# Kernel tuning notes

Hardware: AMD Instinct MI355X
Metric: run time of the kernel (lower is better)

The kernel has to match this reference:

```python
import jax, jax.numpy as jnp
import numpy as np

IRREPS = [(32, 0), (16, 1), (8, 2)]          # (multiplicity, l)
DIMS = [m * (2 * l + 1) for m, l in IRREPS]  # [32, 48, 40]
OFF = np.concatenate([[0], np.cumsum(DIMS)]).astype(int)
FEAT = int(OFF[-1])                          # 120
H = 4                                        # num_heads
EPS = 1e-5
N_NODES = 50000
N_EDGES = 800000


def split(x):
    # split last axis into per-irrep blocks [..., mul, 2l+1]
    return [x[..., OFF[i]:OFF[i + 1]].reshape(x.shape[:-1] + (m, 2 * l + 1))
            for i, (m, l) in enumerate(IRREPS)]


def merge(blocks, lead):
    return jnp.concatenate([b.reshape(lead + (-1,)) for b in blocks], axis=-1)


def o3_linear(x, Ws):
    # e3nn o3.Linear: mixes multiplicities within each irrep type, 1/sqrt(fan_in) norm
    bs = split(x)
    out = [jnp.einsum('...im,io->...om', b, W) / np.sqrt(m)
           for b, W, (m, l) in zip(bs, Ws, IRREPS)]
    return merge(out, x.shape[:-1])


def norm_act(x):
    # e3nn nn.NormActivation with sigmoid: y = sigmoid(|x|) * x / |x| per irrep
    out = []
    for b in split(x):
        n = jnp.sqrt(jnp.sum(b * b, axis=-1, keepdims=True) + EPS * EPS)
        out.append(jax.nn.sigmoid(n) * b / n)
    return merge(out, x.shape[:-1])


def tp_dot(q, k, Wd):
    # FullyConnectedTensorProduct(q_ir, k_ir, 'Hx0e'), component normalization:
    # per-edge weighted inner products between matching irreps -> [E, H]
    fan = sum(m * m * (2 * l + 1) for m, l in IRREPS)
    out = 0.0
    for qb, kb, W, (m, l) in zip(split(q), split(k), Wd, IRREPS):
        out = out + jnp.einsum('eim,ejm,ijh->eh', qb, kb, W) / np.sqrt(2 * l + 1)
    return out / np.sqrt(fan)


def setup_inputs() -> dict:
    key = jax.random.key(0)
    ks = jax.random.split(key, 16)
    inp = {"node_features": jax.random.normal(ks[0], (N_NODES, FEAT), jnp.float32)}
    i = 1
    for name in ("Wq", "Wk", "Wv"):
        for j, (m, l) in enumerate(IRREPS):
            inp[f"{name}{j}"] = jax.random.normal(ks[i], (m, m), jnp.float32); i += 1
    for j, (m, l) in enumerate(IRREPS):
        inp[f"Wd{j}"] = jax.random.normal(ks[i], (m, m, H), jnp.float32); i += 1
    inp["edge_dst"] = jax.random.randint(ks[i], (N_EDGES,), 0, N_NODES); i += 1
    inp["edge_src"] = jax.random.randint(ks[i], (N_EDGES,), 0, N_NODES)
    return inp


def reference(node_features, Wq0, Wq1, Wq2, Wk0, Wk1, Wk2, Wv0, Wv1, Wv2,
              Wd0, Wd1, Wd2, edge_dst, edge_src):
    N = node_features.shape[0]
    q = norm_act(o3_linear(node_features, [Wq0, Wq1, Wq2]))              # [N, F]
    k = norm_act(o3_linear(node_features[edge_src], [Wk0, Wk1, Wk2]))    # [E, F]
    v_node = norm_act(o3_linear(node_features, [Wv0, Wv1, Wv2]))         # [N, F]
    v = v_node[edge_src]                                                 # [E, F]
    exp = jnp.exp(tp_dot(q[edge_dst], k, [Wd0, Wd1, Wd2]))               # [E, H]
    exp = jnp.mean(exp, axis=1, keepdims=True)                           # [E, 1]
    z = jax.ops.segment_sum(exp, edge_dst, num_segments=N)               # [N, 1]
    z = jnp.where(z == 0, 1.0, z)
    alpha = exp / z[edge_dst]                                            # [E, 1]
    f_out = jax.ops.segment_sum(jnp.sqrt(jax.nn.relu(alpha)) * v,
                                edge_dst, num_segments=N)                # [N, F]
    return f_out + v_node
```

## Files before the change

kernel.cpp:

```cpp
#include <hip/hip_runtime.h>
#include <math.h>

#define FEAT 120
#define HCNT 4

typedef unsigned short ushort_t;
typedef unsigned int uint_t;
typedef __attribute__((ext_vector_type(8))) short short8;
typedef __attribute__((ext_vector_type(4))) float floatx4;

__device__ __forceinline__ float nact_scale(float sumsq) {
    float n = sqrtf(sumsq + 1e-10f);
    float sig = 1.0f / (1.0f + expf(-n));
    return sig / n;
}

__device__ __forceinline__ ushort_t bf16r(float f) {
    uint_t u = __float_as_uint(f);
    u += 0x7fff + ((u >> 16) & 1);
    return (ushort_t)(u >> 16);
}

__device__ __forceinline__ uint_t pack2(float lo, float hi) {
    return (uint_t)bf16r(lo) | ((uint_t)bf16r(hi) << 16);
}

#define INV_S32 0.17677669529663687f
#define INV_S16 0.25f
#define INV_S8  0.35355339059327373f
#define S_IR0 0.02175970668223486f
#define S_IR1 0.012562972567021898f
#define S_IR2 0.009731317442393031f


__global__ __launch_bounds__(256) void zero_int_kernel(int* __restrict__ p, int n) {
    int i = blockIdx.x * 256 + threadIdx.x;
    if (i < n) p[i] = 0;
}

__global__ __launch_bounds__(256) void hist_kernel(const int* __restrict__ dst,
                                                   int* __restrict__ cnt, int E) {
    int e = blockIdx.x * 256 + threadIdx.x;
    if (e < E) atomicAdd(&cnt[dst[e]], 1);
}

__global__ __launch_bounds__(256) void scan_block_kernel(const int* __restrict__ cnt,
                                                         int* __restrict__ excl,
                                                         int* __restrict__ bsum, int n) {
    __shared__ int s[256];
    int t = threadIdx.x;
    int i = blockIdx.x * 256 + t;
    int v = (i < n) ? cnt[i] : 0;
    s[t] = v;
    __syncthreads();
    for (int off = 1; off < 256; off <<= 1) {
        int add = (t >= off) ? s[t - off] : 0;
        __syncthreads();
        s[t] += add;
        __syncthreads();
    }
    if (i < n) excl[i] = s[t] - v;
    if (t == 255) bsum[blockIdx.x] = s[255];
}

__global__ __launch_bounds__(256) void scan_sums_kernel(int* __restrict__ bsum, int nb) {
    __shared__ int s[256];
    int t = threadIdx.x;
    int v = (t < nb) ? bsum[t] : 0;
    s[t] = v;
    __syncthreads();
    for (int off = 1; off < 256; off <<= 1) {
        int add = (t >= off) ? s[t - off] : 0;
        __syncthreads();
        s[t] += add;
        __syncthreads();
    }
    if (t < nb) bsum[t] = s[t] - v;
}

__global__ __launch_bounds__(256) void add_offsets_kernel(int* __restrict__ offsets,
                                                          const int* __restrict__ bsum,
                                                          int* __restrict__ cursor,
                                                          int n, int E) {
    int i = blockIdx.x * 256 + threadIdx.x;
    if (i < n) {
        int off = offsets[i] + bsum[i >> 8];
        offsets[i] = off;
        cursor[i] = off;
    }
    if (i == 0) offsets[n] = E;
}

__global__ __launch_bounds__(256) void scatter_kernel(const int* __restrict__ dst,
                                                      const int* __restrict__ src,
                                                      int* __restrict__ cursor,
                                                      int* __restrict__ ssrc, int E) {
    int e = blockIdx.x * 256 + threadIdx.x;
    if (e < E) {
        int pos = atomicAdd(&cursor[dst[e]], 1);
        ssrc[pos] = src[e];
    }
}


__global__ __launch_bounds__(256) void prep_zero_kernel(uint_t* __restrict__ p, int nwords) {
    int i = blockIdx.x * 256 + threadIdx.x;
    if (i < nwords) p[i] = 0;
}

__global__ __launch_bounds__(256) void prep_fill_kernel(
    const float* __restrict__ Wq0, const float* __restrict__ Wq1, const float* __restrict__ Wq2,
    const float* __restrict__ Wk0, const float* __restrict__ Wk1, const float* __restrict__ Wk2,
    const float* __restrict__ Wv0, const float* __restrict__ Wv1, const float* __restrict__ Wv2,
    const float* __restrict__ Wd0, const float* __restrict__ Wd1, const float* __restrict__ Wd2,
    float* __restrict__ wt, ushort_t* __restrict__ wdtb)
{
    int t = threadIdx.x;
    for (int it = t; it < 3072; it += 256) {
        int p = it >> 10, rem = it & 1023, o = rem >> 5, i = rem & 31;
        const float* W = (p == 0) ? Wq0 : (p == 1) ? Wk0 : Wv0;
        wt[p * 1344 + o * 32 + i] = W[i * 32 + o] * INV_S32;
    }
    for (int it = t; it < 768; it += 256) {
        int p = it >> 8, rem = it & 255, o = rem >> 4, i = rem & 15;
        const float* W = (p == 0) ? Wq1 : (p == 1) ? Wk1 : Wv1;
        wt[p * 1344 + 1024 + o * 16 + i] = W[i * 16 + o] * INV_S16;
    }
    for (int it = t; it < 192; it += 256) {
        int p = it / 64, rem = it % 64, o = rem >> 3, i = rem & 7;
        const float* W = (p == 0) ? Wq2 : (p == 1) ? Wk2 : Wv2;
        wt[p * 1344 + 1280 + o * 8 + i] = W[i * 8 + o] * INV_S8;
    }
    for (int it = t; it < 4096; it += 256) {
        int i = it / 128, rem = it % 128, j = rem / 4, h = rem % 4;
        wdtb[(h * 128 + j) * 128 + i] = bf16r(Wd0[i * 128 + j * 4 + h] * S_IR0);
    }
    for (int it = t; it < 3072; it += 256) {
        int i = it / 192, rem = it % 192, j = rem / 12, r2 = rem % 12, c = r2 / 4, h = r2 % 4;
        wdtb[(h * 128 + 32 + j * 3 + c) * 128 + (32 + i * 3 + c)] = bf16r(Wd1[i * 64 + j * 4 + h] * S_IR1);
    }
    for (int it = t; it < 1280; it += 256) {
        int i = it / 160, rem = it % 160, j = rem / 20, r2 = rem % 20, c = r2 / 4, h = r2 % 4;
        wdtb[(h * 128 + 80 + j * 5 + c) * 128 + (80 + i * 5 + c)] = bf16r(Wd2[i * 32 + j * 4 + h] * S_IR2);
    }
}


__global__ __launch_bounds__(256) void node_qkv_v5_kernel(
    const float* __restrict__ x, const float* __restrict__ wt,
    ushort_t* __restrict__ S0q, ushort_t* __restrict__ S1q, ushort_t* __restrict__ S2q,
    ushort_t* __restrict__ S0k, ushort_t* __restrict__ S1k, ushort_t* __restrict__ S2k,
    ushort_t* __restrict__ S0v, ushort_t* __restrict__ S1v, ushort_t* __restrict__ S2v,
    int N)
{
    int node = blockIdx.x * 256 + threadIdx.x;
    int p = blockIdx.y;
    int sec = blockIdx.z;
    if (node >= N) return;

    const float4* xp = (const float4*)(x + (size_t)node * FEAT);
    const float* W = wt + p * 1344;

    if (sec == 0) {
        float xs[32];
        #pragma unroll
        for (int i = 0; i < 8; i++) ((float4*)xs)[i] = xp[i];
        uint_t yp[16];
        float prev = 0.0f;
        #pragma unroll
        for (int o = 0; o < 32; o++) {
            float acc = 0.0f;
            const float* w0 = W + o * 32;
            #pragma unroll
            for (int i = 0; i < 32; i++) acc = fmaf(w0[i], xs[i], acc);
            float y = acc * nact_scale(acc * acc);
            if (o & 1) yp[o >> 1] = pack2(prev, y); else prev = y;
        }
        ushort_t* D = (p == 0) ? S0q : (p == 1) ? S0k : S0v;
        uint4* dst = (uint4*)(D + (size_t)node * 32);
        #pragma unroll
        for (int i = 0; i < 4; i++)
            dst[i] = (uint4){yp[4*i], yp[4*i+1], yp[4*i+2], yp[4*i+3]};
    } else if (sec == 1) {
        float xs[48];
        #pragma unroll
        for (int i = 0; i < 12; i++) ((float4*)xs)[i] = xp[8 + i];
        uint_t yp[24];
        float prev = 0.0f;
        #pragma unroll
        for (int o = 0; o < 16; o++) {
            float a0 = 0.0f, a1 = 0.0f, a2 = 0.0f;
            const float* w1 = W + 1024 + o * 16;
            #pragma unroll
            for (int i = 0; i < 16; i++) {
                float w = w1[i];
                a0 = fmaf(w, xs[i * 3 + 0], a0);
                a1 = fmaf(w, xs[i * 3 + 1], a1);
                a2 = fmaf(w, xs[i * 3 + 2], a2);
            }
            float s = nact_scale(a0 * a0 + a1 * a1 + a2 * a2);
            float y0 = a0 * s, y1 = a1 * s, y2 = a2 * s;
            int f = o * 3;
            if (f & 1) {
                yp[f >> 1] = pack2(prev, y0);
                yp[(f >> 1) + 1] = pack2(y1, y2);
            } else {
                yp[f >> 1] = pack2(y0, y1);
                prev = y2;
            }
        }
        ushort_t* D = (p == 0) ? S1q : (p == 1) ? S1k : S1v;
        uint4* dst = (uint4*)(D + (size_t)node * 48);
        #pragma unroll
        for (int i = 0; i < 6; i++)
            dst[i] = (uint4){yp[4*i], yp[4*i+1], yp[4*i+2], yp[4*i+3]};
    } else {
        float xs[40];
        #pragma unroll
        for (int i = 0; i < 10; i++) ((float4*)xs)[i] = xp[20 + i];
        uint_t yp[20];
        float prev = 0.0f;
        #pragma unroll
        for (int o = 0; o < 8; o++) {
            float a0 = 0, a1 = 0, a2 = 0, a3 = 0, a4 = 0;
            const float* w2 = W + 1280 + o * 8;
            #pragma unroll
            for (int i = 0; i < 8; i++) {
                float w = w2[i];
                a0 = fmaf(w, xs[i * 5 + 0], a0);
                a1 = fmaf(w, xs[i * 5 + 1], a1);
                a2 = fmaf(w, xs[i * 5 + 2], a2);
                a3 = fmaf(w, xs[i * 5 + 3], a3);
                a4 = fmaf(w, xs[i * 5 + 4], a4);
            }
            float s = nact_scale(a0*a0 + a1*a1 + a2*a2 + a3*a3 + a4*a4);
            float y0 = a0*s, y1 = a1*s, y2 = a2*s, y3 = a3*s, y4 = a4*s;
            int f = o * 5;
            if (f & 1) {
                yp[f >> 1] = pack2(prev, y0);
                yp[(f >> 1) + 1] = pack2(y1, y2);
                yp[(f >> 1) + 2] = pack2(y3, y4);
            } else {
                yp[f >> 1] = pack2(y0, y1);
                yp[(f >> 1) + 1] = pack2(y2, y3);
                prev = y4;
            }
        }
        ushort_t* D = (p == 0) ? S2q : (p == 1) ? S2k : S2v;
        uint4* dst = (uint4*)(D + (size_t)node * 48);
        #pragma unroll
        for (int i = 0; i < 5; i++)
            dst[i] = (uint4){yp[4*i], yp[4*i+1], yp[4*i+2], yp[4*i+3]};
        dst[5] = (uint4){0, 0, 0, 0};
    }
}



__global__ __launch_bounds__(256, 2) void node_tq_mfma_kernel(
    const ushort_t* __restrict__ S0q, const ushort_t* __restrict__ S1q,
    const ushort_t* __restrict__ S2q, const ushort_t* __restrict__ wdtb,
    ushort_t* __restrict__ tqb, int N)
{
    int t = threadIdx.x, lane = t & 63, w = t >> 6;
    int base = blockIdx.x * 16;
    int nl = lane & 15, quad = lane >> 4, q8 = quad * 8;
    int node = base + nl;
    int nclamp = (node < N) ? node : (N - 1);

    size_t r32 = (size_t)nclamp * 32, r48 = (size_t)nclamp * 48;
    short8 bfr[4];
    bfr[0] = *(const short8*)(S0q + r32 + q8);
    bfr[1] = *(const short8*)(S1q + r48 + q8);
    bfr[2] = (quad < 2) ? *(const short8*)(S1q + r48 + 32 + q8)
                        : *(const short8*)(S2q + r48 + q8 - 16);
    bfr[3] = *(const short8*)(S2q + r48 + 16 + q8);

    #pragma unroll
    for (int ti = 0; ti < 8; ti++) {
        int tile = w * 8 + ti;
        const ushort_t* ap = wdtb + (tile * 16 + nl) * 128 + q8;
        floatx4 C = {0.0f, 0.0f, 0.0f, 0.0f};
        #pragma unroll
        for (int kk = 0; kk < 4; kk++) {
            short8 a = *(const short8*)(ap + kk * 32);
            C = __builtin_amdgcn_mfma_f32_16x16x32_bf16(a, bfr[kk], C, 0, 0, 0);
        }
        if (node < N) {
            uint_t lo = (uint_t)bf16r(C[0]) | ((uint_t)bf16r(C[1]) << 16);
            uint_t hi = (uint_t)bf16r(C[2]) | ((uint_t)bf16r(C[3]) << 16);
            uint_t* dst = (uint_t*)(tqb + (size_t)node * 512 + tile * 16 + quad * 4);
            dst[0] = lo; dst[1] = hi;
        }
    }
}


__global__ __launch_bounds__(256) void edge_mfma_kernel(
    const ushort_t* __restrict__ tqb,
    const ushort_t* __restrict__ S0k, const ushort_t* __restrict__ S1k,
    const ushort_t* __restrict__ S2k,
    const ushort_t* __restrict__ S0v, const ushort_t* __restrict__ S1v,
    const ushort_t* __restrict__ S2v,
    const int* __restrict__ offsets, const int* __restrict__ ssrc,
    float* __restrict__ out, int N)
{
    int lane = threadIdx.x & 63, wid = threadIdx.x >> 6;
    int node = blockIdx.x * 4 + wid;
    if (node >= N) return;
    node = __builtin_amdgcn_readfirstlane(node);
    int m = lane & 15, quad = lane >> 4, q8 = quad * 8;

    short8 afr[4];
    if (m < HCNT) {
        const short8* ap = (const short8*)(tqb + (size_t)node * 512 + m * 128 + q8);
        #pragma unroll
        for (int b = 0; b < 4; b++) afr[b] = ap[b * 4];
    } else {
        #pragma unroll
        for (int b = 0; b < 4; b++) afr[b] = (short8){0,0,0,0,0,0,0,0};
    }

    const ushort_t* c2base = (quad < 2) ? S1k : S2k;
    int c2off = (quad < 2) ? 32 + q8 : q8 - 16;

    const uint_t* vb0 = (const uint_t*)S0v;
    const uint_t* vb1 = (const uint_t*)S1v;
    const uint_t* vb2 = (const uint_t*)S2v;
    const uint_t* vbase = (lane < 16) ? vb0 : (lane < 40) ? vb1 : vb2;
    int vstride = (lane < 16) ? 16 : 24;
    int voff = (lane < 16) ? lane : (lane < 40) ? lane - 16 : lane - 40;

    int beg = offsets[node], end = offsets[node + 1];
    float zpart = 0.0f, accx = 0.0f, accy = 0.0f;

    for (int tb = beg; tb < end; tb += 16) {
        int rem = end - tb; if (rem > 16) rem = 16;
        int idx = tb + (m < rem ? m : rem - 1);
        int src = ssrc[idx];
        size_t r32 = (size_t)src * 32, r48 = (size_t)src * 48;
        short8 b0 = *(const short8*)(S0k + r32 + q8);
        short8 b1 = *(const short8*)(S1k + r48 + q8);
        short8 b2 = *(const short8*)(c2base + r48 + c2off);
        short8 b3 = *(const short8*)(S2k + r48 + 16 + q8);
        floatx4 C = {0.0f, 0.0f, 0.0f, 0.0f};
        C = __builtin_amdgcn_mfma_f32_16x16x32_bf16(afr[0], b0, C, 0, 0, 0);
        C = __builtin_amdgcn_mfma_f32_16x16x32_bf16(afr[1], b1, C, 0, 0, 0);
        C = __builtin_amdgcn_mfma_f32_16x16x32_bf16(afr[2], b2, C, 0, 0, 0);
        C = __builtin_amdgcn_mfma_f32_16x16x32_bf16(afr[3], b3, C, 0, 0, 0);

        float w = 0.0f;
        if (quad == 0 && m < rem) {
            float ex = 0.25f * (__expf(C[0]) + __expf(C[1]) + __expf(C[2]) + __expf(C[3]));
            zpart += ex;
            w = sqrtf(ex);
        }

        if (rem == 16) {
            #pragma unroll
            for (int e0 = 0; e0 < 16; e0 += 8) {
                float we[8]; int se[8]; uint_t vp[8];
                #pragma unroll
                for (int j = 0; j < 8; j++) {
                    we[j] = __shfl(w, e0 + j, 64);
                    se[j] = __shfl(src, e0 + j, 64);
                }
                #pragma unroll
                for (int j = 0; j < 8; j++)
                    vp[j] = vbase[(size_t)se[j] * vstride + voff];
                #pragma unroll
                for (int j = 0; j < 8; j++) {
                    accx = fmaf(we[j], __uint_as_float(vp[j] << 16), accx);
                    accy = fmaf(we[j], __uint_as_float(vp[j] & 0xffff0000u), accy);
                }
            }
        } else {
            for (int e = 0; e < rem; e++) {
                float we = __shfl(w, e, 64);
                int   se = __shfl(src, e, 64);
                uint_t vp = vbase[(size_t)se * vstride + voff];
                accx = fmaf(we, __uint_as_float(vp << 16), accx);
                accy = fmaf(we, __uint_as_float(vp & 0xffff0000u), accy);
            }
        }
    }

    zpart += __shfl_xor(zpart, 1, 64);
    zpart += __shfl_xor(zpart, 2, 64);
    zpart += __shfl_xor(zpart, 4, 64);
    zpart += __shfl_xor(zpart, 8, 64);
    float zsum = __shfl(zpart, 0, 64);
    float scale = (zsum > 0.0f) ? rsqrtf(zsum) : 0.0f;

    if (lane < 60) {
        uint_t vself = vbase[(size_t)node * vstride + voff];
        float2 o;
        o.x = fmaf(accx, scale, __uint_as_float(vself << 16));
        o.y = fmaf(accy, scale, __uint_as_float(vself & 0xffff0000u));
        *((float2*)(out + (size_t)node * FEAT) + lane) = o;
    }
}


extern "C" void kernel_launch(void* const* d_in, const int* in_sizes, int n_in,
                              void* d_out, int out_size, void* d_ws, size_t ws_size,
                              hipStream_t stream) {
    const float* x   = (const float*)d_in[0];
    const float* Wq0 = (const float*)d_in[1];
    const float* Wq1 = (const float*)d_in[2];
    const float* Wq2 = (const float*)d_in[3];
    const float* Wk0 = (const float*)d_in[4];
    const float* Wk1 = (const float*)d_in[5];
    const float* Wk2 = (const float*)d_in[6];
    const float* Wv0 = (const float*)d_in[7];
    const float* Wv1 = (const float*)d_in[8];
    const float* Wv2 = (const float*)d_in[9];
    const float* Wd0 = (const float*)d_in[10];
    const float* Wd1 = (const float*)d_in[11];
    const float* Wd2 = (const float*)d_in[12];
    const int* edge_dst = (const int*)d_in[13];
    const int* edge_src = (const int*)d_in[14];
    float* out = (float*)d_out;

    int N = in_sizes[0] / FEAT;
    int E = in_sizes[13];

    ushort_t* S0q = (ushort_t*)d_ws;
    ushort_t* S1q = S0q + (size_t)N * 32;
    ushort_t* S2q = S1q + (size_t)N * 48;
    ushort_t* S0k = S2q + (size_t)N * 48;
    ushort_t* S1k = S0k + (size_t)N * 32;
    ushort_t* S2k = S1k + (size_t)N * 48;
    ushort_t* S0v = S2k + (size_t)N * 48;
    ushort_t* S1v = S0v + (size_t)N * 32;
    ushort_t* S2v = S1v + (size_t)N * 48;
    ushort_t* tqb = S2v + (size_t)N * 48;
    ushort_t* wdtb = tqb + (size_t)N * 512;
    float* wt      = (float*)(wdtb + 65536);
    int* offsets = (int*)(wt + 4032);
    int* cursor  = offsets + (N + 1);
    int* bsum    = cursor + N;
    int* ssrc    = bsum + 256;

    int NB = (N + 255) / 256;
    int EB = (E + 255) / 256;
    int NW = (N + 3) / 4;
    int NT = (N + 15) / 16;

    prep_zero_kernel<<<128, 256, 0, stream>>>((uint_t*)wdtb, 32768);
    prep_fill_kernel<<<1, 256, 0, stream>>>(Wq0, Wq1, Wq2, Wk0, Wk1, Wk2,
                                            Wv0, Wv1, Wv2, Wd0, Wd1, Wd2, wt, wdtb);

    zero_int_kernel<<<NB, 256, 0, stream>>>(cursor, N);
    hist_kernel<<<EB, 256, 0, stream>>>(edge_dst, cursor, E);
    scan_block_kernel<<<NB, 256, 0, stream>>>(cursor, offsets, bsum, N);
    scan_sums_kernel<<<1, 256, 0, stream>>>(bsum, NB);
    add_offsets_kernel<<<NB, 256, 0, stream>>>(offsets, bsum, cursor, N, E);
    scatter_kernel<<<EB, 256, 0, stream>>>(edge_dst, edge_src, cursor, ssrc, E);

    node_qkv_v5_kernel<<<dim3(NB, 3, 3), 256, 0, stream>>>(
        x, wt, S0q, S1q, S2q, S0k, S1k, S2k, S0v, S1v, S2v, N);
    node_tq_mfma_kernel<<<NT, 256, 0, stream>>>(S0q, S1q, S2q, wdtb, tqb, N);
    edge_mfma_kernel<<<NW, 256, 0, stream>>>(tqb, S0k, S1k, S2k, S0v, S1v, S2v,
                                             offsets, ssrc, out, N);
}
```

Baseline: 407.3 us.

## Interleave K and V rows per node and unroll edge loop by two tiles

The node tq kernel now also copies the split per-irrep K and V bf16 arrays into contiguous 128-element rows per node. The edge kernel then gathers each source's K and V from a single 256-byte row instead of three separate arrays. The edge loop handles 32 edges per iteration with two independent MFMA chains to hide gather latency, leaving a 16-edge tail loop. Two zeroing kernels are also folded into prep_fill and a memset to cut launches, at the cost of an extra copy pass and more workspace.

```diff
diff --git a/kernel.cpp b/kernel.cpp
--- a/kernel.cpp
+++ b/kernel.cpp
@@ -32,11 +32,6 @@
 #define S_IR1 0.012562972567021898f
 #define S_IR2 0.009731317442393031f
 
-
-__global__ __launch_bounds__(256) void zero_int_kernel(int* __restrict__ p, int n) {
-    int i = blockIdx.x * 256 + threadIdx.x;
-    if (i < n) p[i] = 0;
-}
 
 __global__ __launch_bounds__(256) void hist_kernel(const int* __restrict__ dst,
                                                    int* __restrict__ cnt, int E) {
@@ -103,11 +98,6 @@
 }
 
 
-__global__ __launch_bounds__(256) void prep_zero_kernel(uint_t* __restrict__ p, int nwords) {
-    int i = blockIdx.x * 256 + threadIdx.x;
-    if (i < nwords) p[i] = 0;
-}
-
 __global__ __launch_bounds__(256) void prep_fill_kernel(
     const float* __restrict__ Wq0, const float* __restrict__ Wq1, const float* __restrict__ Wq2,
     const float* __restrict__ Wk0, const float* __restrict__ Wk1, const float* __restrict__ Wk2,
@@ -116,6 +106,8 @@
     float* __restrict__ wt, ushort_t* __restrict__ wdtb)
 {
     int t = threadIdx.x;
+    for (int it = t; it < 32768; it += 256) ((uint_t*)wdtb)[it] = 0;
+    __syncthreads();
     for (int it = t; it < 3072; it += 256) {
         int p = it >> 10, rem = it & 1023, o = rem >> 5, i = rem & 31;
         const float* W = (p == 0) ? Wq0 : (p == 1) ? Wk0 : Wv0;
@@ -256,14 +248,37 @@
 }
 
 
-
 __global__ __launch_bounds__(256, 2) void node_tq_mfma_kernel(
     const ushort_t* __restrict__ S0q, const ushort_t* __restrict__ S1q,
-    const ushort_t* __restrict__ S2q, const ushort_t* __restrict__ wdtb,
-    ushort_t* __restrict__ tqb, int N)
+    const ushort_t* __restrict__ S2q,
+    const ushort_t* __restrict__ S0k, const ushort_t* __restrict__ S1k,
+    const ushort_t* __restrict__ S2k,
+    const ushort_t* __restrict__ S0v, const ushort_t* __restrict__ S1v,
+    const ushort_t* __restrict__ S2v,
+    const ushort_t* __restrict__ wdtb,
+    ushort_t* __restrict__ tqb, ushort_t* __restrict__ kb, ushort_t* __restrict__ vb,
+    int N)
 {
     int t = threadIdx.x, lane = t & 63, w = t >> 6;
     int base = blockIdx.x * 16;
+
+    {
+        int rn = t >> 4, c = t & 15;
+        int node2 = base + rn;
+        if (node2 < N) {
+            size_t r32 = (size_t)node2 * 32, r48 = (size_t)node2 * 48;
+            uint4 kv, vv;
+            if (c < 4)       { kv = *(const uint4*)(S0k + r32 + c * 8);
+                               vv = *(const uint4*)(S0v + r32 + c * 8); }
+            else if (c < 10) { kv = *(const uint4*)(S1k + r48 + (c - 4) * 8);
+                               vv = *(const uint4*)(S1v + r48 + (c - 4) * 8); }
+            else             { kv = *(const uint4*)(S2k + r48 + (c - 10) * 8);
+                               vv = *(const uint4*)(S2v + r48 + (c - 10) * 8); }
+            *(uint4*)(kb + (size_t)node2 * 128 + c * 8) = kv;
+            *(uint4*)(vb + (size_t)node2 * 128 + c * 8) = vv;
+        }
+    }
+
     int nl = lane & 15, quad = lane >> 4, q8 = quad * 8;
     int node = base + nl;
     int nclamp = (node < N) ? node : (N - 1);
@@ -297,11 +312,8 @@
 
 
 __global__ __launch_bounds__(256) void edge_mfma_kernel(
-    const ushort_t* __restrict__ tqb,
-    const ushort_t* __restrict__ S0k, const ushort_t* __restrict__ S1k,
-    const ushort_t* __restrict__ S2k,
-    const ushort_t* __restrict__ S0v, const ushort_t* __restrict__ S1v,
-    const ushort_t* __restrict__ S2v,
+    const ushort_t* __restrict__ tqb, const ushort_t* __restrict__ kb,
+    const ushort_t* __restrict__ vb,
     const int* __restrict__ offsets, const int* __restrict__ ssrc,
     float* __restrict__ out, int N)
 {
@@ -321,67 +333,82 @@
         for (int b = 0; b < 4; b++) afr[b] = (short8){0,0,0,0,0,0,0,0};
     }
 
-    const ushort_t* c2base = (quad < 2) ? S1k : S2k;
-    int c2off = (quad < 2) ? 32 + q8 : q8 - 16;
-
-    const uint_t* vb0 = (const uint_t*)S0v;
-    const uint_t* vb1 = (const uint_t*)S1v;
-    const uint_t* vb2 = (const uint_t*)S2v;
-    const uint_t* vbase = (lane < 16) ? vb0 : (lane < 40) ? vb1 : vb2;
-    int vstride = (lane < 16) ? 16 : 24;
-    int voff = (lane < 16) ? lane : (lane < 40) ? lane - 16 : lane - 40;
-
     int beg = offsets[node], end = offsets[node + 1];
     float zpart = 0.0f, accx = 0.0f, accy = 0.0f;
-
-    for (int tb = beg; tb < end; tb += 16) {
-        int rem = end - tb; if (rem > 16) rem = 16;
-        int idx = tb + (m < rem ? m : rem - 1);
-        int src = ssrc[idx];
-        size_t r32 = (size_t)src * 32, r48 = (size_t)src * 48;
-        short8 b0 = *(const short8*)(S0k + r32 + q8);
-        short8 b1 = *(const short8*)(S1k + r48 + q8);
-        short8 b2 = *(const short8*)(c2base + r48 + c2off);
-        short8 b3 = *(const short8*)(S2k + r48 + 16 + q8);
-        floatx4 C = {0.0f, 0.0f, 0.0f, 0.0f};
-        C = __builtin_amdgcn_mfma_f32_16x16x32_bf16(afr[0], b0, C, 0, 0, 0);
-        C = __builtin_amdgcn_mfma_f32_16x16x32_bf16(afr[1], b1, C, 0, 0, 0);
-        C = __builtin_amdgcn_mfma_f32_16x16x32_bf16(afr[2], b2, C, 0, 0, 0);
-        C = __builtin_amdgcn_mfma_f32_16x16x32_bf16(afr[3], b3, C, 0, 0, 0);
-
-        float w = 0.0f;
-        if (quad == 0 && m < rem) {
-            float ex = 0.25f * (__expf(C[0]) + __expf(C[1]) + __expf(C[2]) + __expf(C[3]));
-            zpart += ex;
-            w = sqrtf(ex);
-        }
-
-        if (rem == 16) {
+    const uint_t* vrow = (const uint_t*)vb;
+
+    int p = beg;
+    for (; p + 32 <= end; p += 32) {
+        int srcA = ssrc[p + m];
+        int srcB = ssrc[p + 16 + m];
+        const short8* bpA = (const short8*)(kb + (size_t)srcA * 128 + q8);
+        const short8* bpB = (const short8*)(kb + (size_t)srcB * 128 + q8);
+        short8 a0 = bpA[0], a1 = bpA[4], a2 = bpA[8], a3 = bpA[12];
+        short8 c0 = bpB[0], c1 = bpB[4], c2 = bpB[8], c3 = bpB[12];
+        floatx4 CA = {0.0f, 0.0f, 0.0f, 0.0f};
+        floatx4 CB = {0.0f, 0.0f, 0.0f, 0.0f};
+        CA = __builtin_amdgcn_mfma_f32_16x16x32_bf16(afr[0], a0, CA, 0, 0, 0);
+        CB = __builtin_amdgcn_mfma_f32_16x16x32_bf16(afr[0], c0, CB, 0, 0, 0);
+        CA = __builtin_amdgcn_mfma_f32_16x16x32_bf16(afr[1], a1, CA, 0, 0, 0);
+        CB = __builtin_amdgcn_mfma_f32_16x16x32_bf16(afr[1], c1, CB, 0, 0, 0);
+        CA = __builtin_amdgcn_mfma_f32_16x16x32_bf16(afr[2], a2, CA, 0, 0, 0);
+        CB = __builtin_amdgcn_mfma_f32_16x16x32_bf16(afr[2], c2, CB, 0, 0, 0);
+        CA = __builtin_amdgcn_mfma_f32_16x16x32_bf16(afr[3], a3, CA, 0, 0, 0);
+        CB = __builtin_amdgcn_mfma_f32_16x16x32_bf16(afr[3], c3, CB, 0, 0, 0);
+
+        float wA = 0.0f, wB = 0.0f;
+        if (quad == 0) {
+            float exA = 0.25f * (__expf(CA[0]) + __expf(CA[1]) + __expf(CA[2]) + __expf(CA[3]));
+            float exB = 0.25f * (__expf(CB[0]) + __expf(CB[1]) + __expf(CB[2]) + __expf(CB[3]));
+            zpart += exA + exB;
+            wA = sqrtf(exA); wB = sqrtf(exB);
+        }
+        #pragma unroll
+        for (int half = 0; half < 2; half++) {
+            float wsel = half ? wB : wA;
+            int ssel = half ? srcB : srcA;
             #pragma unroll
             for (int e0 = 0; e0 < 16; e0 += 8) {
                 float we[8]; int se[8]; uint_t vp[8];
                 #pragma unroll
                 for (int j = 0; j < 8; j++) {
-                    we[j] = __shfl(w, e0 + j, 64);
-                    se[j] = __shfl(src, e0 + j, 64);
+                    we[j] = __shfl(wsel, e0 + j, 64);
+                    se[j] = __shfl(ssel, e0 + j, 64);
                 }
                 #pragma unroll
-                for (int j = 0; j < 8; j++)
-                    vp[j] = vbase[(size_t)se[j] * vstride + voff];
+                for (int j = 0; j < 8; j++) vp[j] = vrow[(size_t)se[j] * 64 + lane];
                 #pragma unroll
                 for (int j = 0; j < 8; j++) {
                     accx = fmaf(we[j], __uint_as_float(vp[j] << 16), accx);
                     accy = fmaf(we[j], __uint_as_float(vp[j] & 0xffff0000u), accy);
                 }
             }
-        } else {
-            for (int e = 0; e < rem; e++) {
-                float we = __shfl(w, e, 64);
-                int   se = __shfl(src, e, 64);
-                uint_t vp = vbase[(size_t)se * vstride + voff];
-                accx = fmaf(we, __uint_as_float(vp << 16), accx);
-                accy = fmaf(we, __uint_as_float(vp & 0xffff0000u), accy);
-            }
+        }
+    }
+    for (; p < end; p += 16) {
+        int rem = end - p; if (rem > 16) rem = 16;
+        int idx = p + (m < rem ? m : rem - 1);
+        int src = ssrc[idx];
+        const short8* bp = (const short8*)(kb + (size_t)src * 128 + q8);
+        short8 b0 = bp[0], b1 = bp[4], b2 = bp[8], b3 = bp[12];
+        floatx4 C = {0.0f, 0.0f, 0.0f, 0.0f};
+        C = __builtin_amdgcn_mfma_f32_16x16x32_bf16(afr[0], b0, C, 0, 0, 0);
+        C = __builtin_amdgcn_mfma_f32_16x16x32_bf16(afr[1], b1, C, 0, 0, 0);
+        C = __builtin_amdgcn_mfma_f32_16x16x32_bf16(afr[2], b2, C, 0, 0, 0);
+        C = __builtin_amdgcn_mfma_f32_16x16x32_bf16(afr[3], b3, C, 0, 0, 0);
+
+        float w = 0.0f;
+        if (quad == 0 && m < rem) {
+            float ex = 0.25f * (__expf(C[0]) + __expf(C[1]) + __expf(C[2]) + __expf(C[3]));
+            zpart += ex;
+            w = sqrtf(ex);
+        }
+        for (int e = 0; e < rem; e++) {
+            float we = __shfl(w, e, 64);
+            int   se = __shfl(src, e, 64);
+            uint_t vp = vrow[(size_t)se * 64 + lane];
+            accx = fmaf(we, __uint_as_float(vp << 16), accx);
+            accy = fmaf(we, __uint_as_float(vp & 0xffff0000u), accy);
         }
     }
 
@@ -393,7 +420,7 @@
     float scale = (zsum > 0.0f) ? rsqrtf(zsum) : 0.0f;
 
     if (lane < 60) {
-        uint_t vself = vbase[(size_t)node * vstride + voff];
+        uint_t vself = vrow[(size_t)node * 64 + lane];
         float2 o;
         o.x = fmaf(accx, scale, __uint_as_float(vself << 16));
         o.y = fmaf(accy, scale, __uint_as_float(vself & 0xffff0000u));
@@ -434,7 +461,9 @@
     ushort_t* S0v = S2k + (size_t)N * 48;
     ushort_t* S1v = S0v + (size_t)N * 32;
     ushort_t* S2v = S1v + (size_t)N * 48;
-    ushort_t* tqb = S2v + (size_t)N * 48;
+    ushort_t* kb  = S2v + (size_t)N * 48;
+    ushort_t* vb  = kb + (size_t)N * 128;
+    ushort_t* tqb = vb + (size_t)N * 128;
     ushort_t* wdtb = tqb + (size_t)N * 512;
     float* wt      = (float*)(wdtb + 65536);
     int* offsets = (int*)(wt + 4032);
@@ -447,11 +476,10 @@
     int NW = (N + 3) / 4;
     int NT = (N + 15) / 16;
 
-    prep_zero_kernel<<<128, 256, 0, stream>>>((uint_t*)wdtb, 32768);
     prep_fill_kernel<<<1, 256, 0, stream>>>(Wq0, Wq1, Wq2, Wk0, Wk1, Wk2,
                                             Wv0, Wv1, Wv2, Wd0, Wd1, Wd2, wt, wdtb);
 
-    zero_int_kernel<<<NB, 256, 0, stream>>>(cursor, N);
+    hipMemsetAsync(cursor, 0, (size_t)N * sizeof(int), stream);
     hist_kernel<<<EB, 256, 0, stream>>>(edge_dst, cursor, E);
     scan_block_kernel<<<NB, 256, 0, stream>>>(cursor, offsets, bsum, N);
     scan_sums_kernel<<<1, 256, 0, stream>>>(bsum, NB);
@@ -460,7 +488,7 @@
 
     node_qkv_v5_kernel<<<dim3(NB, 3, 3), 256, 0, stream>>>(
         x, wt, S0q, S1q, S2q, S0k, S1k, S2k, S0v, S1v, S2v, N);
-    node_tq_mfma_kernel<<<NT, 256, 0, stream>>>(S0q, S1q, S2q, wdtb, tqb, N);
-    edge_mfma_kernel<<<NW, 256, 0, stream>>>(tqb, S0k, S1k, S2k, S0v, S1v, S2v,
-                                             offsets, ssrc, out, N);
-}
+    node_tq_mfma_kernel<<<NT, 256, 0, stream>>>(S0q, S1q, S2q, S0k, S1k, S2k,
+                                                S0v, S1v, S2v, wdtb, tqb, kb, vb, N);
+    edge_mfma_kernel<<<NW, 256, 0, stream>>>(tqb, kb, vb, offsets, ssrc, out, N);
+}
```

Measured after the change: 433.0 us. +6.3%, slower.
